# Kernel tuning notes

Measured on AMD Instinct MI355X. Metric: run time of the kernel, lower is better.

The kernel has to match this reference:

```python
import jax, jax.numpy as jnp
import numpy as np

NUM_CLASSES = 200
NUM_FEATURES = 128
NUM_PROTO_PER_CLASS = 10
NUM_PROTOTYPES = NUM_CLASSES * NUM_PROTO_PER_CLASS
EPS = 1e-4
INCORRECT_STRENGTH = -0.5


def _make_last_layer_weight():
    # prototype_class_identity[j, j // num_proto_per_class] = 1; weight = correct + (-0.5)*incorrect
    proto_ids = np.arange(NUM_PROTOTYPES) // NUM_PROTO_PER_CLASS  # (P,)
    correct = (np.arange(NUM_CLASSES)[:, None] == proto_ids[None, :]).astype(np.float32)  # (C, P)
    weight = correct + INCORRECT_STRENGTH * (1.0 - correct)
    return jnp.asarray(weight)


def setup_inputs() -> dict:
    key = jax.random.key(0)
    k1, k2 = jax.random.split(key)
    features = jax.random.normal(k1, (64, NUM_FEATURES, 14, 14), dtype=jnp.float32)
    # SHIFTED_NORMAL prototype init: small-variance normal shifted by 0.5
    prototypes = 0.5 + 0.1 * jax.random.normal(k2, (NUM_PROTOTYPES, NUM_FEATURES, 1, 1), dtype=jnp.float32)
    last_weight = _make_last_layer_weight()  # (C, P)
    return {"features": features, "prototypes": prototypes, "last_weight": last_weight}


def reference(features, prototypes, last_weight):
    # features: (N, D, H, W); prototypes: (P, D, 1, 1); last_weight: (C, P)
    protos = prototypes[:, :, 0, 0]  # (P, D)
    x_sq = jnp.sum(features * features, axis=1, keepdims=True)  # (N, 1, H, W)
    p_sq = jnp.sum(protos * protos, axis=1)  # (P,)
    xp = jnp.einsum("ndhw,pd->nphw", features, protos)  # (N, P, H, W)
    dist = jax.nn.relu(x_sq + p_sq[None, :, None, None] - 2.0 * xp)  # (N, P, H, W)
    sim = jnp.log((dist + 1.0) / (dist + EPS))  # (N, P, H, W)
    sim_max = jnp.max(sim.reshape(sim.shape[0], sim.shape[1], -1), axis=2)  # (N, P)
    logits = sim_max @ last_weight.T  # (N, C)
    min_dist = jnp.min(dist.reshape(dist.shape[0], dist.shape[1], -1), axis=2)  # (N, P)
    return (logits, min_dist)
```

## Files before the change

### kernel.cpp

```cpp
#include <hip/hip_runtime.h>
#include <hip/hip_bf16.h>

#define NUM_CLASSES 200
#define NF 128
#define NP 2000
#define NPC 10
#define HW 196
#define MPAD 208
#define NCH 13
#define NB 64
#define EPSV 1e-4f
#define TROW 17
#define PTILE 500
#define CTILE 50

typedef __attribute__((ext_vector_type(8))) short short8;
typedef __attribute__((ext_vector_type(4))) float f32x4;

static __device__ __forceinline__ unsigned short f2bf(float x) {
    __hip_bfloat16 h = __float2bfloat16(x);
    return __builtin_bit_cast(unsigned short, h);
}

__global__ __launch_bounds__(512, 2) void kmain(const float* __restrict__ f,
                                                const float* __restrict__ protos,
                                                const float* __restrict__ W,
                                                float* __restrict__ min_out,
                                                float* __restrict__ logits) {
    __shared__ unsigned short sf[MPAD * NF];
    __shared__ float tile[2][NF * TROW];
    __shared__ float sxsq[MPAD];
    __shared__ float scsum[64];
    float* const ssim = (float*)sf;

    const int n    = blockIdx.x;
    const int pt   = blockIdx.y;
    const int t    = threadIdx.x;
    const int wave = t >> 6;
    const int lane = t & 63;
    const int row  = lane & 15;
    const int quad = lane >> 4;
    const int sb   = wave * 64;
    const int p0   = pt * PTILE;

    short8 A[4][4];
    float psum[4];
    #pragma unroll
    for (int g = 0; g < 4; ++g) {
        int p = p0 + sb + g * 16 + row;
        const float* ap = protos + (size_t)(p < NP ? p : NP - 1) * NF + quad * 8;
        psum[g] = 0.f;
        #pragma unroll
        for (int kk = 0; kk < 4; ++kk) {
            float4 w0 = *(const float4*)(ap + kk * 32);
            float4 w1 = *(const float4*)(ap + kk * 32 + 4);
            psum[g] += w0.x * w0.x + w0.y * w0.y + w0.z * w0.z + w0.w * w0.w
                     + w1.x * w1.x + w1.y * w1.y + w1.z * w1.z + w1.w * w1.w;
            short8 a;
            a[0] = (short)f2bf(w0.x); a[1] = (short)f2bf(w0.y);
            a[2] = (short)f2bf(w0.z); a[3] = (short)f2bf(w0.w);
            a[4] = (short)f2bf(w1.x); a[5] = (short)f2bf(w1.y);
            a[6] = (short)f2bf(w1.z); a[7] = (short)f2bf(w1.w);
            A[g][kk] = a;
        }
        psum[g] += __shfl_xor(psum[g], 16, 64);
        psum[g] += __shfl_xor(psum[g], 32, 64);
    }

    const int tl   = t & 255;
    const int ch   = t >> 8;
    const int kb   = tl >> 2;
    const int hwl  = (tl & 3) * 4;
    const int hwl2 = tl >> 4;
    const int kg   = tl & 15;

    for (int rd = 0; rd < 7; ++rd) {
        const int mt  = rd * 2 + ch;
        const int hw0 = mt * 16;
        float4 v0 = make_float4(0.f, 0.f, 0.f, 0.f), v1 = v0;
        if (mt < NCH && hw0 + hwl + 4 <= HW) {
            v0 = *(const float4*)(f + ((size_t)n * NF + kb) * HW + hw0 + hwl);
            v1 = *(const float4*)(f + ((size_t)n * NF + kb + 64) * HW + hw0 + hwl);
        }
        __syncthreads();
        if (mt < NCH) {
            tile[ch][kb * TROW + hwl + 0] = v0.x;
            tile[ch][kb * TROW + hwl + 1] = v0.y;
            tile[ch][kb * TROW + hwl + 2] = v0.z;
            tile[ch][kb * TROW + hwl + 3] = v0.w;
            tile[ch][(kb + 64) * TROW + hwl + 0] = v1.x;
            tile[ch][(kb + 64) * TROW + hwl + 1] = v1.y;
            tile[ch][(kb + 64) * TROW + hwl + 2] = v1.z;
            tile[ch][(kb + 64) * TROW + hwl + 3] = v1.w;
        }
        __syncthreads();
        if (mt < NCH) {
            float xp = 0.f;
            unsigned short u[8];
            #pragma unroll
            for (int j = 0; j < 8; ++j) {
                float val = tile[ch][(kg * 8 + j) * TROW + hwl2];
                xp += val * val;
                u[j] = f2bf(val);
            }
            ((uint4*)sf)[(hw0 + hwl2) * 16 + (kg ^ hwl2)] = *(uint4*)u;
            xp += __shfl_xor(xp, 1, 64);
            xp += __shfl_xor(xp, 2, 64);
            xp += __shfl_xor(xp, 4, 64);
            xp += __shfl_xor(xp, 8, 64);
            if (kg == 0) sxsq[hw0 + hwl2] = (hw0 + hwl2 < HW) ? xp : 3.0e38f;
        }
    }
    __syncthreads();

    float runmin[4][4];
    #pragma unroll
    for (int g = 0; g < 4; ++g)
        #pragma unroll
        for (int r = 0; r < 4; ++r) runmin[g][r] = 3.0e38f;

    const short8* sfv = (const short8*)sf;
    for (int mt = 0; mt < NCH; ++mt) {
        const int base = (mt * 16 + row) * 16;
        short8 b0 = sfv[base + ((quad + 0)  ^ row)];
        short8 b1 = sfv[base + ((quad + 4)  ^ row)];
        short8 b2 = sfv[base + ((quad + 8)  ^ row)];
        short8 b3 = sfv[base + ((quad + 12) ^ row)];
        float xv = sxsq[mt * 16 + row];

        #pragma unroll
        for (int g = 0; g < 4; ++g) {
            f32x4 acc = {0.f, 0.f, 0.f, 0.f};
            acc = __builtin_amdgcn_mfma_f32_16x16x32_bf16(A[g][0], b0, acc, 0, 0, 0);
            acc = __builtin_amdgcn_mfma_f32_16x16x32_bf16(A[g][1], b1, acc, 0, 0, 0);
            acc = __builtin_amdgcn_mfma_f32_16x16x32_bf16(A[g][2], b2, acc, 0, 0, 0);
            acc = __builtin_amdgcn_mfma_f32_16x16x32_bf16(A[g][3], b3, acc, 0, 0, 0);
            #pragma unroll
            for (int r = 0; r < 4; ++r)
                runmin[g][r] = fminf(runmin[g][r], xv - 2.f * acc[r]);
        }
    }

    __syncthreads();

    #pragma unroll
    for (int g = 0; g < 4; ++g) {
        #pragma unroll
        for (int off = 1; off < 16; off <<= 1)
            #pragma unroll
            for (int r = 0; r < 4; ++r)
                runmin[g][r] = fminf(runmin[g][r], __shfl_xor(runmin[g][r], off, 64));
        #pragma unroll
        for (int r = 0; r < 4; ++r) {
            float psq_sel = __shfl(psum[g], 20 * quad + r, 64);
            int slot = sb + g * 16 + quad * 4 + r;
            if (row == 0) {
                float sim = 0.f;
                if (slot < PTILE) {
                    float m = fmaxf(runmin[g][r] + psq_sel, 0.f);
                    min_out[(size_t)n * NP + p0 + slot] = m;
                    sim = logf((m + 1.f) / (m + EPSV));
                }
                ssim[slot] = sim;
            }
        }
    }
    __syncthreads();

    if (t < CTILE) {
        float s = 0.f;
        #pragma unroll
        for (int j = 0; j < NPC; ++j) s += ssim[t * NPC + j];
        scsum[t] = s;
    }
    __syncthreads();

    if (t < NUM_CLASSES) {
        const float a = W[0];
        const float b = W[NPC];
        float tp = 0.f;
        #pragma unroll
        for (int j = 0; j < CTILE; ++j) tp += scsum[j];
        float v = b * tp;
        const int c0 = pt * CTILE;
        if (t >= c0 && t < c0 + CTILE) v += (a - b) * scsum[t - c0];
        atomicAdd(&logits[(size_t)n * NUM_CLASSES + t], v);
    }
}

extern "C" void kernel_launch(void* const* d_in, const int* in_sizes, int n_in,
                              void* d_out, int out_size, void* d_ws, size_t ws_size,
                              hipStream_t stream) {
    const float* f      = (const float*)d_in[0];
    const float* protos = (const float*)d_in[1];
    const float* W      = (const float*)d_in[2];

    float* logits   = (float*)d_out;
    float* min_dist = (float*)d_out + NB * NUM_CLASSES;

    (void)d_ws; (void)ws_size;

    hipMemsetAsync(logits, 0, (size_t)NB * NUM_CLASSES * sizeof(float), stream);
    kmain<<<dim3(NB, 4), 512, 0, stream>>>(f, protos, W, min_dist, logits);
}
```

Baseline: 82.48 us.

## Load features directly into bf16 LDS layout, dropping transpose tile and extra syncs

Replaces the 7-round staged transpose through a padded fp32 LDS tile with a direct load. Each thread reads 8 channels by 2 spatial positions as float2, converts them to bf16 and writes them straight into the swizzled LDS operand layout. Per-thread partial squared norms go to a small LDS buffer and are reduced by 208 threads afterwards. The feature loads are also issued before the prototype register loads so the two can overlap. This removes about 14 block barriers and the fp32 round trip through LDS, at the cost of narrower float2 global loads and a strided partial-sum reduction.

```diff
diff --git a/kernel.cpp b/kernel.cpp
--- a/kernel.cpp
+++ b/kernel.cpp
@@ -10,7 +10,6 @@
 #define NCH 13
 #define NB 64
 #define EPSV 1e-4f
-#define TROW 17
 #define PTILE 500
 #define CTILE 50
 
@@ -28,7 +27,7 @@
                                                 float* __restrict__ min_out,
                                                 float* __restrict__ logits) {
     __shared__ unsigned short sf[MPAD * NF];
-    __shared__ float tile[2][NF * TROW];
+    __shared__ float swp[16 * MPAD];
     __shared__ float sxsq[MPAD];
     __shared__ float scsum[64];
     float* const ssim = (float*)sf;
@@ -42,6 +41,36 @@
     const int quad = lane >> 4;
     const int sb   = wave * 64;
     const int p0   = pt * PTILE;
+
+    const int kg = t >> 5;
+    const int rp = t & 31;
+    const float* fkg = f + ((size_t)n * NF + kg * 8) * HW;
+    #pragma unroll
+    for (int rd = 0; rd < 4; ++rd) {
+        const int hw = rd * 64 + rp * 2;
+        float2 v[8];
+        if (hw + 2 <= HW) {
+            #pragma unroll
+            for (int j = 0; j < 8; ++j)
+                v[j] = *(const float2*)(fkg + j * HW + hw);
+        } else {
+            #pragma unroll
+            for (int j = 0; j < 8; ++j) v[j] = make_float2(0.f, 0.f);
+        }
+        if (hw < MPAD) {
+            unsigned short u0[8], u1[8];
+            float s0 = 0.f, s1 = 0.f;
+            #pragma unroll
+            for (int j = 0; j < 8; ++j) {
+                s0 += v[j].x * v[j].x;  s1 += v[j].y * v[j].y;
+                u0[j] = f2bf(v[j].x);   u1[j] = f2bf(v[j].y);
+            }
+            ((uint4*)sf)[hw * 16       + (kg ^ (hw & 15))]       = *(uint4*)u0;
+            ((uint4*)sf)[(hw + 1) * 16 + (kg ^ ((hw + 1) & 15))] = *(uint4*)u1;
+            swp[kg * MPAD + hw]     = s0;
+            swp[kg * MPAD + hw + 1] = s1;
+        }
+    }
 
     short8 A[4][4];
     float psum[4];
@@ -67,49 +96,13 @@
         psum[g] += __shfl_xor(psum[g], 32, 64);
     }
 
-    const int tl   = t & 255;
-    const int ch   = t >> 8;
-    const int kb   = tl >> 2;
-    const int hwl  = (tl & 3) * 4;
-    const int hwl2 = tl >> 4;
-    const int kg   = tl & 15;
+    __syncthreads();
 
-    for (int rd = 0; rd < 7; ++rd) {
-        const int mt  = rd * 2 + ch;
-        const int hw0 = mt * 16;
-        float4 v0 = make_float4(0.f, 0.f, 0.f, 0.f), v1 = v0;
-        if (mt < NCH && hw0 + hwl + 4 <= HW) {
-            v0 = *(const float4*)(f + ((size_t)n * NF + kb) * HW + hw0 + hwl);
-            v1 = *(const float4*)(f + ((size_t)n * NF + kb + 64) * HW + hw0 + hwl);
-        }
-        __syncthreads();
-        if (mt < NCH) {
-            tile[ch][kb * TROW + hwl + 0] = v0.x;
-            tile[ch][kb * TROW + hwl + 1] = v0.y;
-            tile[ch][kb * TROW + hwl + 2] = v0.z;
-            tile[ch][kb * TROW + hwl + 3] = v0.w;
-            tile[ch][(kb + 64) * TROW + hwl + 0] = v1.x;
-            tile[ch][(kb + 64) * TROW + hwl + 1] = v1.y;
-            tile[ch][(kb + 64) * TROW + hwl + 2] = v1.z;
-            tile[ch][(kb + 64) * TROW + hwl + 3] = v1.w;
-        }
-        __syncthreads();
-        if (mt < NCH) {
-            float xp = 0.f;
-            unsigned short u[8];
-            #pragma unroll
-            for (int j = 0; j < 8; ++j) {
-                float val = tile[ch][(kg * 8 + j) * TROW + hwl2];
-                xp += val * val;
-                u[j] = f2bf(val);
-            }
-            ((uint4*)sf)[(hw0 + hwl2) * 16 + (kg ^ hwl2)] = *(uint4*)u;
-            xp += __shfl_xor(xp, 1, 64);
-            xp += __shfl_xor(xp, 2, 64);
-            xp += __shfl_xor(xp, 4, 64);
-            xp += __shfl_xor(xp, 8, 64);
-            if (kg == 0) sxsq[hw0 + hwl2] = (hw0 + hwl2 < HW) ? xp : 3.0e38f;
-        }
+    if (t < MPAD) {
+        float s = 0.f;
+        #pragma unroll
+        for (int g16 = 0; g16 < 16; ++g16) s += swp[g16 * MPAD + t];
+        sxsq[t] = (t < HW) ? s : 3.0e38f;
     }
     __syncthreads();
 
```

Measured after the change: 79.71 us. 1.03x faster.
